# Kernel tuning notes

Hardware: AMD Instinct MI355X
Metric: run time of the kernel (lower is better)

The kernel has to match this reference:

```python
import jax, jax.numpy as jnp
import numpy as np

NUM_USERS, NUM_ITEMS, RANK = 610, 193609, 4
BATCH = 2097152


def setup_inputs() -> dict:
    key = jax.random.key(0)
    ks = jax.random.split(key, 10)
    users = jax.random.randint(ks[0], (BATCH,), 0, NUM_USERS + 1)
    items = jax.random.randint(ks[1], (BATCH,), 0, NUM_ITEMS + 1)
    # embedding tables (nn.Embedding default init ~ N(0,1))
    embed_U = jax.random.normal(ks[2], (NUM_USERS + 1, RANK), dtype=jnp.float32)
    embed_V = jax.random.normal(ks[3], (NUM_ITEMS + 1, RANK), dtype=jnp.float32)
    # Linear params, Kaiming-uniform-ish scale (1/sqrt(fan_in))
    def lin(k, fan_in, fan_out):
        k1, k2 = jax.random.split(k)
        bound = 1.0 / np.sqrt(fan_in)
        W = jax.random.uniform(k1, (fan_out, fan_in), jnp.float32, -bound, bound)
        b = jax.random.uniform(k2, (fan_out,), jnp.float32, -bound, bound)
        return W, b
    W1, b1 = lin(ks[4], 2 * RANK, 50)
    W2, b2 = lin(ks[5], 50, 20)
    W3, b3 = lin(ks[6], 20, 1)
    return {"users": users, "items": items,
            "embed_U": embed_U, "embed_V": embed_V,
            "W1": W1, "b1": b1, "W2": W2, "b2": b2, "W3": W3, "b3": b3}


def reference(users, items, embed_U, embed_V, W1, b1, W2, b2, W3, b3):
    # Vectorized version of the per-sample loop: gather + concat + 3-layer MLP
    eu = embed_U[users]                      # [B, rank]
    ev = embed_V[items]                      # [B, rank]
    x = jnp.concatenate([eu, ev], axis=-1)   # [B, 2*rank]
    x = jax.nn.relu(x @ W1.T + b1)           # [B, 50]
    x = jax.nn.relu(x @ W2.T + b2)           # [B, 20]
    x = x @ W3.T + b3                        # [B, 1]
    return x[:, 0]                           # [B]
```

## Files before the change

kernel.cpp:

```cpp
#include <hip/hip_runtime.h>
#include <hip/hip_fp16.h>


typedef __attribute__((ext_vector_type(16))) float    f32x16;
typedef __attribute__((ext_vector_type(8)))  _Float16 f16x8;
typedef __attribute__((ext_vector_type(2)))  __fp16   h16x2;

#define H1 50
#define H2 20
#define NUSERS 611

union W4 { unsigned u[4]; f16x8 v; };
union W8 { _Float16 h[8]; f16x8 v; };

static __device__ inline unsigned pk_u32(float a, float b) {
    h16x2 p = __builtin_amdgcn_cvt_pkrtz(a, b);
    unsigned u; __builtin_memcpy(&u, &p, 4); return u;
}
static __device__ inline unsigned pkmax0(unsigned a) {
    unsigned r;
    asm("v_pk_max_f16 %0, %1, %2" : "=v"(r) : "v"(a), "v"(0u));
    return r;
}

__global__ __launch_bounds__(256) void neumf_mfma32(
    const int* __restrict__ users, const int* __restrict__ items,
    const float* __restrict__ eU, const float* __restrict__ eV,
    const float* __restrict__ W1, const float* __restrict__ b1,
    const float* __restrict__ W2, const float* __restrict__ b2,
    const float* __restrict__ W3, const float* __restrict__ b3,
    float* __restrict__ out, int n, int nTiles, int tilesPerWave)
{
    const int lane = threadIdx.x & 63;
    const int wid  = blockIdx.x * (blockDim.x >> 6) + (threadIdx.x >> 6);
    const int h    = lane >> 5;
    const int r31  = lane & 31;

    __shared__ float4 ldsU[NUSERS];
    for (int r = threadIdx.x; r < NUSERS; r += 256)
        ldsU[r] = reinterpret_cast<const float4*>(eU)[r];
    __syncthreads();

    f16x8 a1[2];
#pragma unroll
    for (int mt = 0; mt < 2; ++mt) {
        int m = 32 * mt + r31;
        float w[8] = {0.f,0.f,0.f,0.f,0.f,0.f,0.f,0.f};
        if (m < H1) {
#pragma unroll
            for (int i = 0; i < 4; ++i) w[i] = W1[m * 8 + 4 * h + i];
            if (h == 0) w[4] = b1[m];
        }
        W8 f;
#pragma unroll
        for (int i = 0; i < 8; ++i) f.h[i] = (_Float16)w[i];
        a1[mt] = f.v;
    }

    f16x8 a2[4];
    {
        int m = r31;
#pragma unroll
        for (int kt = 0; kt < 4; ++kt) {
            float w[8] = {0.f,0.f,0.f,0.f,0.f,0.f,0.f,0.f};
            if (m < H2) {
#pragma unroll
                for (int e = 0; e < 8; ++e) {
                    int k = 16 * kt + 4 * h + (e & 3) + 8 * (e >> 2);
                    if (k < H1)       w[e] = W2[m * H1 + k];
                    else if (k == H1) w[e] = b2[m];
                }
            }
            W8 f;
#pragma unroll
            for (int e = 0; e < 8; ++e) f.h[e] = (_Float16)w[e];
            a2[kt] = f.v;
        }
    }

    f16x8 a3;
    {
        W8 f;
#pragma unroll
        for (int e = 0; e < 8; ++e) {
            int k = 4 * h + (e & 3) + 8 * (e >> 2);
            f.h[e] = (_Float16)W3[k];
        }
        a3 = f.v;
    }
    float w3t[4];
#pragma unroll
    for (int j = 0; j < 4; ++j) w3t[j] = h ? 0.f : W3[16 + j];
    const float bias3 = b3[0];

    const int*     ip  = h ? items : users;
    const unsigned w2c = h ? 0u : 0x00003C00u;

    const int t0 = wid * tilesPerWave;
    const int t1 = min(t0 + tilesPerWave, nTiles);
    if (t0 >= t1) return;

    int idx_cur = ip[32 * t0 + r31];
    float4 gv_cur = *reinterpret_cast<const float4*>(eV + 4 * (size_t)(h ? idx_cur : 0));
    int idx_next = ip[32 * min(t0 + 1, t1 - 1) + r31];

    for (int T = t0; T < t1; ++T) {
        float4 gv_next = *reinterpret_cast<const float4*>(eV + 4 * (size_t)(h ? idx_next : 0));
        int idx_nn = ip[32 * min(T + 2, t1 - 1) + r31];

        float4 lv = ldsU[h ? 0 : idx_cur];
        float4 cur;
        cur.x = h ? gv_cur.x : lv.x;  cur.y = h ? gv_cur.y : lv.y;
        cur.z = h ? gv_cur.z : lv.z;  cur.w = h ? gv_cur.w : lv.w;

        W4 bf1;
        bf1.u[0] = pk_u32(cur.x, cur.y);
        bf1.u[1] = pk_u32(cur.z, cur.w);
        bf1.u[2] = w2c;
        bf1.u[3] = 0u;

        f32x16 z = {0.f,0.f,0.f,0.f,0.f,0.f,0.f,0.f,0.f,0.f,0.f,0.f,0.f,0.f,0.f,0.f};
        f32x16 d1[2];
        d1[0] = __builtin_amdgcn_mfma_f32_32x32x16_f16(a1[0], bf1.v, z, 0, 0, 0);
        d1[1] = __builtin_amdgcn_mfma_f32_32x32x16_f16(a1[1], bf1.v, z, 0, 0, 0);

        d1[1][10] = h ? d1[1][10] : 1.0f;

        f32x16 d2 = z;
#pragma unroll
        for (int kt = 0; kt < 4; ++kt) {
            const int mt = kt >> 1, q = kt & 1;
            W4 bf;
#pragma unroll
            for (int j = 0; j < 4; ++j)
                bf.u[j] = pkmax0(pk_u32(d1[mt][8 * q + 2 * j], d1[mt][8 * q + 2 * j + 1]));
            d2 = __builtin_amdgcn_mfma_f32_32x32x16_f16(a2[kt], bf.v, d2, 0, 0, 0);
        }

        W4 b3f;
        b3f.u[0] = pkmax0(pk_u32(d2[0], d2[1]));
        b3f.u[1] = pkmax0(pk_u32(d2[2], d2[3]));
        b3f.u[2] = pkmax0(pk_u32(d2[4], d2[5]));
        b3f.u[3] = pkmax0(pk_u32(d2[6], d2[7]));
        f32x16 d3 = __builtin_amdgcn_mfma_f32_32x32x16_f16(a3, b3f.v, z, 0, 0, 0);

        float pt = bias3;
#pragma unroll
        for (int j = 0; j < 4; ++j)
            pt = fmaf(fmaxf(d2[8 + j], 0.f), w3t[j], pt);

        float p = d3[0] + pt;
        if (!h) out[32 * T + r31] = p;

        gv_cur = gv_next; idx_cur = idx_next; idx_next = idx_nn;
    }
}

extern "C" void kernel_launch(void* const* d_in, const int* in_sizes, int n_in,
                              void* d_out, int out_size, void* d_ws, size_t ws_size,
                              hipStream_t stream) {
    const int*   users = (const int*)d_in[0];
    const int*   items = (const int*)d_in[1];
    const float* eU    = (const float*)d_in[2];
    const float* eV    = (const float*)d_in[3];
    const float* W1    = (const float*)d_in[4];
    const float* b1    = (const float*)d_in[5];
    const float* W2    = (const float*)d_in[6];
    const float* b2    = (const float*)d_in[7];
    const float* W3    = (const float*)d_in[8];
    const float* b3    = (const float*)d_in[9];
    float*       out   = (float*)d_out;

    int n = in_sizes[0];
    int nTiles = (n + 31) / 32;
    int blocks = 2048, threads = 256;
    int totalWaves = blocks * (threads / 64);
    int tilesPerWave = (nTiles + totalWaves - 1) / totalWaves;
    neumf_mfma32<<<blocks, threads, 0, stream>>>(users, items, eU, eV,
                                                 W1, b1, W2, b2, W3, b3,
                                                 out, n, nTiles, tilesPerWave);
}
```

Measured before the change: 28.32 us.

## Pre-convert embedding tables to packed fp16 and gather 8-byte rows

Adds a prep kernel that converts both embedding tables to packed fp16 pairs in the workspace on every call. The main MFMA kernel then gathers 8-byte rows instead of 16-byte float4 rows and skips the per-sample pack conversion, and the user table is staged in LDS at half the size. The intent is to cut gather bytes and cache traffic in the main kernel. The cost is an extra launch that reads and rewrites the whole item table each call. A scalar VALU fallback kernel is added for when the workspace is too small or the user table too large.

```diff
diff --git a/kernel.cpp b/kernel.cpp
--- a/kernel.cpp
+++ b/kernel.cpp
@@ -8,7 +8,6 @@
 
 #define H1 50
 #define H2 20
-#define NUSERS 611
 
 union W4 { unsigned u[4]; f16x8 v; };
 union W8 { _Float16 h[8]; f16x8 v; };
@@ -23,22 +22,37 @@
     return r;
 }
 
+__global__ __launch_bounds__(256) void prep_f16(
+    const float* __restrict__ eU, const float* __restrict__ eV,
+    uint2* __restrict__ wsU, uint2* __restrict__ wsV, int nU, int nV)
+{
+    int i = blockIdx.x * blockDim.x + threadIdx.x;
+    if (i < nV) {
+        float4 r = reinterpret_cast<const float4*>(eV)[i];
+        wsV[i] = make_uint2(pk_u32(r.x, r.y), pk_u32(r.z, r.w));
+    }
+    if (i < nU) {
+        float4 r = reinterpret_cast<const float4*>(eU)[i];
+        wsU[i] = make_uint2(pk_u32(r.x, r.y), pk_u32(r.z, r.w));
+    }
+}
+
 __global__ __launch_bounds__(256) void neumf_mfma32(
     const int* __restrict__ users, const int* __restrict__ items,
-    const float* __restrict__ eU, const float* __restrict__ eV,
+    const uint2* __restrict__ wsU, const uint2* __restrict__ wsV,
     const float* __restrict__ W1, const float* __restrict__ b1,
     const float* __restrict__ W2, const float* __restrict__ b2,
     const float* __restrict__ W3, const float* __restrict__ b3,
-    float* __restrict__ out, int n, int nTiles, int tilesPerWave)
+    float* __restrict__ out, int n, int nTiles, int tilesPerWave, int nU)
 {
     const int lane = threadIdx.x & 63;
     const int wid  = blockIdx.x * (blockDim.x >> 6) + (threadIdx.x >> 6);
     const int h    = lane >> 5;
     const int r31  = lane & 31;
 
-    __shared__ float4 ldsU[NUSERS];
-    for (int r = threadIdx.x; r < NUSERS; r += 256)
-        ldsU[r] = reinterpret_cast<const float4*>(eU)[r];
+    __shared__ uint2 ldsU[640];
+    for (int r = threadIdx.x; r < nU; r += 256)
+        ldsU[r] = wsU[r];
     __syncthreads();
 
     f16x8 a1[2];
@@ -101,21 +115,22 @@
     if (t0 >= t1) return;
 
     int idx_cur = ip[32 * t0 + r31];
-    float4 gv_cur = *reinterpret_cast<const float4*>(eV + 4 * (size_t)(h ? idx_cur : 0));
+    uint2 gv_cur;
+    if (h) gv_cur = wsV[idx_cur];
     int idx_next = ip[32 * min(t0 + 1, t1 - 1) + r31];
 
     for (int T = t0; T < t1; ++T) {
-        float4 gv_next = *reinterpret_cast<const float4*>(eV + 4 * (size_t)(h ? idx_next : 0));
+        uint2 gv_next;
+        if (h) gv_next = wsV[idx_next];
         int idx_nn = ip[32 * min(T + 2, t1 - 1) + r31];
 
-        float4 lv = ldsU[h ? 0 : idx_cur];
-        float4 cur;
-        cur.x = h ? gv_cur.x : lv.x;  cur.y = h ? gv_cur.y : lv.y;
-        cur.z = h ? gv_cur.z : lv.z;  cur.w = h ? gv_cur.w : lv.w;
+        uint2 cur;
+        if (h) cur = gv_cur;
+        else   cur = ldsU[idx_cur];
 
         W4 bf1;
-        bf1.u[0] = pk_u32(cur.x, cur.y);
-        bf1.u[1] = pk_u32(cur.z, cur.w);
+        bf1.u[0] = cur.x;
+        bf1.u[1] = cur.y;
         bf1.u[2] = w2c;
         bf1.u[3] = 0u;
 
@@ -149,11 +164,44 @@
         for (int j = 0; j < 4; ++j)
             pt = fmaf(fmaxf(d2[8 + j], 0.f), w3t[j], pt);
 
-        float p = d3[0] + pt;
-        if (!h) out[32 * T + r31] = p;
+        if (!h) out[32 * T + r31] = d3[0] + pt;
 
         gv_cur = gv_next; idx_cur = idx_next; idx_next = idx_nn;
     }
+}
+
+__global__ __launch_bounds__(256) void neumf_valu(
+    const int* __restrict__ users, const int* __restrict__ items,
+    const float* __restrict__ eU, const float* __restrict__ eV,
+    const float* __restrict__ W1, const float* __restrict__ b1,
+    const float* __restrict__ W2, const float* __restrict__ b2,
+    const float* __restrict__ W3, const float* __restrict__ b3,
+    float* __restrict__ out, int n)
+{
+    int i = blockIdx.x * blockDim.x + threadIdx.x;
+    if (i >= n) return;
+    float4 xu = *reinterpret_cast<const float4*>(eU + 4 * (size_t)users[i]);
+    float4 xv = *reinterpret_cast<const float4*>(eV + 4 * (size_t)items[i]);
+    float x[8] = {xu.x,xu.y,xu.z,xu.w,xv.x,xv.y,xv.z,xv.w};
+    float h1[H1], h2[H2];
+#pragma unroll
+    for (int j = 0; j < H1; ++j) {
+        float a = b1[j];
+#pragma unroll
+        for (int k = 0; k < 8; ++k) a = fmaf(x[k], W1[j*8+k], a);
+        h1[j] = fmaxf(a, 0.f);
+    }
+#pragma unroll
+    for (int j = 0; j < H2; ++j) {
+        float a = b2[j];
+#pragma unroll
+        for (int k = 0; k < H1; ++k) a = fmaf(h1[k], W2[j*H1+k], a);
+        h2[j] = fmaxf(a, 0.f);
+    }
+    float o = b3[0];
+#pragma unroll
+    for (int k = 0; k < H2; ++k) o = fmaf(h2[k], W3[k], o);
+    out[i] = o;
 }
 
 extern "C" void kernel_launch(void* const* d_in, const int* in_sizes, int n_in,
@@ -171,12 +219,28 @@
     const float* b3    = (const float*)d_in[9];
     float*       out   = (float*)d_out;
 
-    int n = in_sizes[0];
+    int n  = in_sizes[0];
+    int nU = in_sizes[2] / 4;
+    int nV = in_sizes[3] / 4;
+
+    size_t offV = 8192;
+    size_t need = offV + (size_t)nV * 8;
+    if (ws_size < need || nU > 640) {
+        neumf_valu<<<(n + 255) / 256, 256, 0, stream>>>(users, items, eU, eV,
+                                                        W1, b1, W2, b2, W3, b3, out, n);
+        return;
+    }
+
+    uint2* wsU = (uint2*)d_ws;
+    uint2* wsV = (uint2*)((char*)d_ws + offV);
+
+    prep_f16<<<(nV + 255) / 256, 256, 0, stream>>>(eU, eV, wsU, wsV, nU, nV);
+
     int nTiles = (n + 31) / 32;
     int blocks = 2048, threads = 256;
     int totalWaves = blocks * (threads / 64);
     int tilesPerWave = (nTiles + totalWaves - 1) / totalWaves;
-    neumf_mfma32<<<blocks, threads, 0, stream>>>(users, items, eU, eV,
+    neumf_mfma32<<<blocks, threads, 0, stream>>>(users, items, wsU, wsV,
                                                  W1, b1, W2, b2, W3, b3,
-                                                 out, n, nTiles, tilesPerWave);
-}
+                                                 out, n, nTiles, tilesPerWave, nU);
+}
```

Result: slower. 34.19 us (+20.7%).
